# Optimization experiments

Hardware: AMD Instinct MI355X
Metric: run time of the kernel (lower is better)

Reference implementation:

```python
import jax, jax.numpy as jnp
import numpy as np


def setup_inputs() -> dict:
    key = jax.random.key(0)
    kq, kk, kv = jax.random.split(key, 3)
    # transpose_batch_sequence=True layout: [seq, batch, heads, head_dim]
    query = jax.random.normal(kq, (2048, 2, 32, 128), dtype=jnp.float32)
    k = jax.random.normal(kk, (2048, 2, 8, 128), dtype=jnp.float32)
    v = jax.random.normal(kv, (2048, 2, 8, 128), dtype=jnp.float32)
    return {"query": query, "key": k, "value": v}


def reference(query, key, value):
    # scale_attn_logits=True
    head_dim = query.shape[-1]
    q = query / jnp.sqrt(jnp.asarray(head_dim, dtype=query.dtype))
    h_q, h_kv = q.shape[-2], key.shape[-2]
    group_size = h_q // h_kv
    # [q, b, h_kv, g, d]
    gq = q.reshape((*q.shape[:2], h_kv, group_size, q.shape[-1]))
    # scores: [b, h_kv, g, q, k]
    attn = jnp.einsum('qbhgd,kbhd->bhgqk', gq, key)
    attn = jax.nn.softmax(attn, axis=-1)
    # output: [q, b, h_kv, g, d] -> [q, b, h_q, d]
    out = jnp.einsum('bhgqk,kbhd->qbhgd', attn, value)
    return out.reshape(query.shape)
```

## Files before the change

kernel.cpp:

```cpp
#include <hip/hip_runtime.h>

#define SEQ   2048
#define NB    2
#define NHQ   32
#define NHKV  8
#define HD    128
#define QTILE 256
#define QW    32
#define KVB   64
#define NWAVE 8
#define SCALE 0.08838834764831845f
#define QSCALE (0.08838834764831845f * 1.4426950408889634f)
#define THRL2 11.5f

#define QSTRIDE (NB * NHQ * HD)
#define KSTRIDE (NB * NHKV * HD)

typedef float f32x4  __attribute__((ext_vector_type(4)));
typedef float f32x16 __attribute__((ext_vector_type(16)));
typedef __bf16 bf16x8 __attribute__((ext_vector_type(8)));
typedef unsigned short ushort8 __attribute__((ext_vector_type(8)));
typedef unsigned int u32;
typedef unsigned int u32x2 __attribute__((ext_vector_type(2)));
typedef unsigned int u32x4 __attribute__((ext_vector_type(4)));

__device__ __forceinline__ unsigned short f2bf(float f) {
    union { float f; unsigned u; } c; c.f = f;
    return (unsigned short)((c.u + 0x7fffu + ((c.u >> 16) & 1u)) >> 16);
}

__device__ __forceinline__ void gload_lds16(const unsigned short* g, unsigned short* l) {
    __builtin_amdgcn_global_load_lds((const __attribute__((address_space(1))) u32*)g,
                                     (__attribute__((address_space(3))) u32*)l, 16, 0, 0);
}

__device__ __forceinline__ float ex2(float x) {
#if __has_builtin(__builtin_amdgcn_exp2f)
    return __builtin_amdgcn_exp2f(x);
#else
    return exp2f(x);
#endif
}

__device__ __forceinline__ u32 cvtpk(float lo, float hi) {
    u32 r;
    asm("v_cvt_pk_bf16_f32 %0, %1, %2" : "=v"(r) : "v"(lo), "v"(hi));
    return r;
}

__device__ __forceinline__ void pl32swap(u32& a, u32& b) {
#if __has_builtin(__builtin_amdgcn_permlane32_swap)
    u32x2 r = __builtin_amdgcn_permlane32_swap(a, b, false, false);
    a = r.x; b = r.y;
#else
    asm("v_permlane32_swap_b32 %0, %1" : "+v"(a), "+v"(b));
#endif
}

template <int B>
__device__ __forceinline__ bf16x8 make_pa(const f32x16 p) {
    u32 w0 = cvtpk(p[B + 0], p[B + 1]);
    u32 w2 = cvtpk(p[B + 4], p[B + 5]);
    pl32swap(w0, w2);
    u32 w1 = cvtpk(p[B + 2], p[B + 3]);
    u32 w3 = cvtpk(p[B + 6], p[B + 7]);
    pl32swap(w1, w3);
    u32x4 v = {w0, w1, w2, w3};
    return __builtin_bit_cast(bf16x8, v);
}

__global__ __launch_bounds__(256) void conv_k(const float* __restrict__ K,
                                              unsigned short* __restrict__ Kws) {
    int idx = blockIdx.x * 256 + threadIdx.x;
    int c  = idx & 15;
    int s  = (idx >> 4) & 2047;
    int bh = idx >> 15;
    int cs = c ^ (s & 7);
    const float* src = K + ((size_t)s * 16 + bh) * 128 + cs * 8;
    float4 f0 = *(const float4*)src;
    float4 f1 = *(const float4*)(src + 4);
    ushort8 u;
    u[0] = f2bf(f0.x); u[1] = f2bf(f0.y); u[2] = f2bf(f0.z); u[3] = f2bf(f0.w);
    u[4] = f2bf(f1.x); u[5] = f2bf(f1.y); u[6] = f2bf(f1.z); u[7] = f2bf(f1.w);
    *(ushort8*)&Kws[((size_t)bh * 2048 + s) * 128 + c * 8] = u;
}

__global__ __launch_bounds__(256) void conv_v(const float* __restrict__ V,
                                              unsigned short* __restrict__ Vt) {
    __shared__ float tile[64][129];
    int t64 = blockIdx.x & 31;
    int bh  = blockIdx.x >> 5;
    int kv0 = t64 * 64;
#pragma unroll
    for (int i = 0; i < 8; ++i) {
        int f4 = i * 256 + threadIdx.x;
        int kv = f4 >> 5, d4 = (f4 & 31) * 4;
        float4 v = *(const float4*)(V + ((size_t)(kv0 + kv) * 16 + bh) * 128 + d4);
        tile[kv][d4] = v.x; tile[kv][d4 + 1] = v.y;
        tile[kv][d4 + 2] = v.z; tile[kv][d4 + 3] = v.w;
    }
    __syncthreads();
#pragma unroll
    for (int i = 0; i < 4; ++i) {
        int lin = i * 256 + threadIdx.x;
        int c = lin & 7, d = lin >> 3;
        int cs = c ^ (d & 7);
        ushort8 u;
#pragma unroll
        for (int j = 0; j < 8; ++j) u[j] = f2bf(tile[cs * 8 + j][d]);
        *(ushort8*)&Vt[((size_t)bh * 128 + d) * 2048 + kv0 + c * 8] = u;
    }
}

__global__ __launch_bounds__(512, 2)
void attn_fwd3(const float* __restrict__ Q, const unsigned short* __restrict__ Kws,
               const unsigned short* __restrict__ Vtws, float* __restrict__ O) {
    __shared__ __align__(16) unsigned char smemc[69632];

    const int tid  = threadIdx.x;
    const int w    = tid >> 6;
    const int lane = tid & 63;
    const int q31  = lane & 31;
    const int h    = lane >> 5;
    const int c7   = q31 & 7;

    const int bid   = blockIdx.x;
    const int qtile = bid & 7;
    const int g     = (bid >> 3) & 3;
    const int b     = (bid >> 5) & 1;
    const int hkv   = bid >> 6;
    const int hq    = hkv * 4 + g;

    const int qrow = qtile * QTILE + w * QW + q31;

    bf16x8 qf[8];
    {
        const float* qp = Q + (size_t)qrow * QSTRIDE + b * (NHQ * HD) + hq * HD;
#pragma unroll
        for (int s = 0; s < 8; ++s) {
            const float* p = qp + (2 * s + h) * 8;
            float4 f0 = *(const float4*)(p);
            float4 f1 = *(const float4*)(p + 4);
            ushort8 u;
            u[0] = f2bf(f0.x * QSCALE); u[1] = f2bf(f0.y * QSCALE);
            u[2] = f2bf(f0.z * QSCALE); u[3] = f2bf(f0.w * QSCALE);
            u[4] = f2bf(f1.x * QSCALE); u[5] = f2bf(f1.y * QSCALE);
            u[6] = f2bf(f1.z * QSCALE); u[7] = f2bf(f1.w * QSCALE);
            qf[s] = __builtin_bit_cast(bf16x8, u);
        }
    }

    u32 kad[8], vad[4];
#pragma unroll
    for (int s = 0; s < 8; ++s)
        kad[s] = q31 * 256 + (((2 * s + h) ^ c7) << 4);
#pragma unroll
    for (int ks = 0; ks < 4; ++ks)
        vad[ks] = 32768 + q31 * 128 + (((2 * ks + h) ^ c7) << 4);

    f32x16 acc[4];
#pragma unroll
    for (int db = 0; db < 4; ++db) acc[db] = (f32x16)0.f;
    float mr = -3e38f, lsum = 0.f;

    const unsigned short* kbh = Kws  + (size_t)(b * 8 + hkv) * 2048 * 128;
    const unsigned short* vbh = Vtws + (size_t)(b * 8 + hkv) * 128 * 2048;

#define STAGE(bufi, tt) do {                                                           \
        const int kv0s = (tt) * KVB;                                                   \
        _Pragma("unroll")                                                              \
        for (int i_ = 0; i_ < 2; ++i_) {                                               \
            const int c_ = w * 2 + i_;                                                 \
            gload_lds16(kbh + (size_t)(kv0s + c_ * 4 + (lane >> 4)) * 128 + (lane & 15) * 8, \
                        (unsigned short*)(smemc + (bufi) * 16384 + c_ * 1024));        \
            gload_lds16(vbh + (size_t)(c_ * 8 + (lane >> 3)) * 2048 + kv0s + (lane & 7) * 8, \
                        (unsigned short*)(smemc + 32768 + (bufi) * 16384 + c_ * 1024)); \
        }                                                                              \
    } while (0)

    STAGE(0, 0);

    for (int t = 0; t < SEQ / KVB; ++t) {
        __syncthreads();
        if (t + 1 < SEQ / KVB) STAGE((t + 1) & 1, t + 1);

        f32x16 sa0 = (f32x16)0.f, sa1 = (f32x16)0.f;
#pragma unroll
        for (int s = 0; s < 8; ++s) {
            bf16x8 k0 = *(const bf16x8*)&smemc[kad[s]];
            bf16x8 k1 = *(const bf16x8*)&smemc[kad[s] + 8192];
            sa0 = __builtin_amdgcn_mfma_f32_32x32x16_bf16(k0, qf[s], sa0, 0, 0, 0);
            sa1 = __builtin_amdgcn_mfma_f32_32x32x16_bf16(k1, qf[s], sa1, 0, 0, 0);
        }

        float m4[4];
#pragma unroll
        for (int r = 0; r < 4; ++r)
            m4[r] = fmaxf(fmaxf(fmaxf(sa0[r], sa0[r + 4]), fmaxf(sa0[r + 8], sa0[r + 12])),
                          fmaxf(fmaxf(sa1[r], sa1[r + 4]), fmaxf(sa1[r + 8], sa1[r + 12])));
        float tm = fmaxf(fmaxf(m4[0], m4[1]), fmaxf(m4[2], m4[3]));
        tm = fmaxf(tm, __shfl_xor(tm, 32));

        if (!__all(tm <= mr + THRL2)) {
            float mn   = fmaxf(mr, tm);
            float corr = ex2(mr - mn);
            lsum *= corr;
#pragma unroll
            for (int db = 0; db < 4; ++db)
#pragma unroll
                for (int r = 0; r < 16; ++r) acc[db][r] *= corr;
            mr = mn;
        }

#pragma unroll
        for (int r = 0; r < 16; ++r) sa0[r] = ex2(sa0[r] - mr);
#pragma unroll
        for (int r = 0; r < 16; ++r) sa1[r] = ex2(sa1[r] - mr);
        float s4[4];
#pragma unroll
        for (int r = 0; r < 4; ++r)
            s4[r] = (sa0[r] + sa0[r + 4]) + (sa0[r + 8] + sa0[r + 12]) +
                    (sa1[r] + sa1[r + 4]) + (sa1[r + 8] + sa1[r + 12]);
        float ps = (s4[0] + s4[1]) + (s4[2] + s4[3]);
        ps += __shfl_xor(ps, 32);
        lsum += ps;

        bf16x8 pa[4];
        pa[0] = make_pa<0>(sa0);
        pa[1] = make_pa<8>(sa0);
        pa[2] = make_pa<0>(sa1);
        pa[3] = make_pa<8>(sa1);

#pragma unroll
        for (int db = 0; db < 4; ++db) {
#pragma unroll
            for (int ks = 0; ks < 4; ++ks) {
                bf16x8 vf = *(const bf16x8*)&smemc[vad[ks] + db * 4096];
                acc[db] = __builtin_amdgcn_mfma_f32_32x32x16_bf16(vf, pa[ks], acc[db], 0, 0, 0);
            }
        }

#pragma unroll
        for (int s = 0; s < 8; ++s) kad[s] ^= 16384;
#pragma unroll
        for (int ks = 0; ks < 4; ++ks) vad[ks] ^= 16384;
    }
#undef STAGE

    __syncthreads();
    float invl = 1.f / lsum;
    float* ep = (float*)(void*)smemc + w * 2176;
    const int qtb = qtile * QTILE + w * QW;
    float* ob = O + b * (NHQ * HD) + hq * HD;

#pragma unroll
    for (int pass = 0; pass < 2; ++pass) {
#pragma unroll
        for (int db2 = 0; db2 < 2; ++db2) {
            const int db = pass * 2 + db2;
#pragma unroll
            for (int r = 0; r < 16; ++r)
                ep[q31 * 68 + db2 * 32 + (r & 3) + 8 * (r >> 2) + 4 * h] = acc[db][r] * invl;
        }
        __syncthreads();
#pragma unroll
        for (int i = 0; i < 8; ++i) {
            const int row = i * 4 + (lane >> 4);
            const int f4  = lane & 15;
            float4 val = *(const float4*)&ep[row * 68 + f4 * 4];
            *(float4*)(ob + (size_t)(qtb + row) * QSTRIDE + pass * 64 + f4 * 4) = val;
        }
        __syncthreads();
    }
}

#define KPAD  136
#define VPAD  72
#define PPAD  72
__global__ __launch_bounds__(512, 2)
void attn_fwd(const float* __restrict__ Q, const float* __restrict__ K,
              const float* __restrict__ V, float* __restrict__ O) {
    __shared__ __align__(16) unsigned short kbuf[KVB * KPAD];
    __shared__ __align__(16) unsigned short vbuf[HD * VPAD];
    __shared__ __align__(16) unsigned short pbuf[NWAVE][16 * PPAD];

    const int tid = threadIdx.x;
    const int w = tid >> 6, lane = tid & 63;
    const int row16 = lane & 15, kg = lane >> 4;
    const int bid = blockIdx.x;
    const int qtile = bid & 7, g = (bid >> 3) & 3, b = (bid >> 5) & 1, hkv = bid >> 6;
    const int hq = hkv * 4 + g;
    const int qbase = qtile * QTILE + w * 32;

    ushort8 qf[2][4];
#pragma unroll
    for (int s = 0; s < 2; ++s) {
        const int qrow = qbase + s * 16 + row16;
        const float* qp = Q + (size_t)qrow * QSTRIDE + b * (NHQ * HD) + hq * HD;
#pragma unroll
        for (int kk = 0; kk < 4; ++kk) {
            const float* p = qp + kk * 32 + kg * 8;
            float4 f0 = *(const float4*)(p);
            float4 f1 = *(const float4*)(p + 4);
            ushort8 u;
            u[0] = f2bf(f0.x * SCALE); u[1] = f2bf(f0.y * SCALE);
            u[2] = f2bf(f0.z * SCALE); u[3] = f2bf(f0.w * SCALE);
            u[4] = f2bf(f1.x * SCALE); u[5] = f2bf(f1.y * SCALE);
            u[6] = f2bf(f1.z * SCALE); u[7] = f2bf(f1.w * SCALE);
            qf[s][kk] = u;
        }
    }
    float m[2][4], lsum[2][4];
    f32x4 acco[2][8];
#pragma unroll
    for (int s = 0; s < 2; ++s)
#pragma unroll
        for (int r = 0; r < 4; ++r) { m[s][r] = -1e30f; lsum[s][r] = 0.f; }
#pragma unroll
    for (int s = 0; s < 2; ++s)
#pragma unroll
        for (int n = 0; n < 8; ++n) acco[s][n] = (f32x4)0.f;

    const float* kb0 = K + b * (NHKV * HD) + hkv * HD;
    const float* vb0 = V + b * (NHKV * HD) + hkv * HD;

    for (int kvt = 0; kvt < SEQ / KVB; ++kvt) {
        const int kv0 = kvt * KVB;
        __syncthreads();
        const float* kb = kb0 + (size_t)kv0 * KSTRIDE;
#pragma unroll
        for (int i = 0; i < 2; ++i) {
            int c = i * 512 + tid;
            int row = c >> 4, c8 = c & 15;
            const float* src = kb + (size_t)row * KSTRIDE + c8 * 8;
            float4 f0 = *(const float4*)(src);
            float4 f1 = *(const float4*)(src + 4);
            ushort8 u;
            u[0] = f2bf(f0.x); u[1] = f2bf(f0.y); u[2] = f2bf(f0.z); u[3] = f2bf(f0.w);
            u[4] = f2bf(f1.x); u[5] = f2bf(f1.y); u[6] = f2bf(f1.z); u[7] = f2bf(f1.w);
            *(ushort8*)&kbuf[row * KPAD + c8 * 8] = u;
        }
        const float* vb = vb0 + (size_t)kv0 * KSTRIDE;
#pragma unroll
        for (int i = 0; i < 4; ++i) {
            int f4i = i * 512 + tid;
            int kv = f4i >> 5, d0 = (f4i & 31) * 4;
            float4 v4 = *(const float4*)(vb + (size_t)kv * KSTRIDE + d0);
            vbuf[(d0 + 0) * VPAD + kv] = f2bf(v4.x);
            vbuf[(d0 + 1) * VPAD + kv] = f2bf(v4.y);
            vbuf[(d0 + 2) * VPAD + kv] = f2bf(v4.z);
            vbuf[(d0 + 3) * VPAD + kv] = f2bf(v4.w);
        }
        __syncthreads();

        f32x4 sa[2][4];
#pragma unroll
        for (int s = 0; s < 2; ++s)
#pragma unroll
            for (int n = 0; n < 4; ++n) sa[s][n] = (f32x4)0.f;
#pragma unroll
        for (int kk = 0; kk < 4; ++kk) {
#pragma unroll
            for (int n = 0; n < 4; ++n) {
                bf16x8 bfr = *(const bf16x8*)&kbuf[(n * 16 + row16) * KPAD + kk * 32 + kg * 8];
                sa[0][n] = __builtin_amdgcn_mfma_f32_16x16x32_bf16(
                    __builtin_bit_cast(bf16x8, qf[0][kk]), bfr, sa[0][n], 0, 0, 0);
                sa[1][n] = __builtin_amdgcn_mfma_f32_16x16x32_bf16(
                    __builtin_bit_cast(bf16x8, qf[1][kk]), bfr, sa[1][n], 0, 0, 0);
            }
        }
#pragma unroll
        for (int s = 0; s < 2; ++s) {
#pragma unroll
            for (int r = 0; r < 4; ++r) {
                float tm = fmaxf(fmaxf(sa[s][0][r], sa[s][1][r]), fmaxf(sa[s][2][r], sa[s][3][r]));
                tm = fmaxf(tm, __shfl_xor(tm, 1, 16));
                tm = fmaxf(tm, __shfl_xor(tm, 2, 16));
                tm = fmaxf(tm, __shfl_xor(tm, 4, 16));
                tm = fmaxf(tm, __shfl_xor(tm, 8, 16));
                float mn = fmaxf(m[s][r], tm);
                float corr = __expf(m[s][r] - mn);
                float ps = 0.f;
                int prow = kg * 4 + r;
#pragma unroll
                for (int n = 0; n < 4; ++n) {
                    float p = __expf(sa[s][n][r] - mn);
                    ps += p;
                    pbuf[w][prow * PPAD + n * 16 + row16] = f2bf(p);
                }
                ps += __shfl_xor(ps, 1, 16);
                ps += __shfl_xor(ps, 2, 16);
                ps += __shfl_xor(ps, 4, 16);
                ps += __shfl_xor(ps, 8, 16);
                lsum[s][r] = lsum[s][r] * corr + ps;
                m[s][r] = mn;
#pragma unroll
                for (int n8 = 0; n8 < 8; ++n8) acco[s][n8][r] *= corr;
            }
#pragma unroll
            for (int kk2 = 0; kk2 < 2; ++kk2) {
                bf16x8 pa = *(const bf16x8*)&pbuf[w][row16 * PPAD + kk2 * 32 + kg * 8];
#pragma unroll
                for (int n8 = 0; n8 < 8; ++n8) {
                    bf16x8 vf = *(const bf16x8*)&vbuf[(n8 * 16 + row16) * VPAD + kk2 * 32 + kg * 8];
                    acco[s][n8] = __builtin_amdgcn_mfma_f32_16x16x32_bf16(pa, vf, acco[s][n8], 0, 0, 0);
                }
            }
        }
    }
    float* ob = O + b * (NHQ * HD) + hq * HD;
#pragma unroll
    for (int s = 0; s < 2; ++s)
#pragma unroll
        for (int r = 0; r < 4; ++r) {
            float inv = 1.f / lsum[s][r];
            int qrow = qbase + s * 16 + kg * 4 + r;
            float* op = ob + (size_t)qrow * QSTRIDE;
#pragma unroll
            for (int n8 = 0; n8 < 8; ++n8)
                op[n8 * 16 + row16] = acco[s][n8][r] * inv;
        }
}

extern "C" void kernel_launch(void* const* d_in, const int* in_sizes, int n_in,
                              void* d_out, int out_size, void* d_ws, size_t ws_size,
                              hipStream_t stream) {
    (void)in_sizes; (void)n_in; (void)out_size;
    const float* Q = (const float*)d_in[0];
    const float* K = (const float*)d_in[1];
    const float* V = (const float*)d_in[2];
    float* Out = (float*)d_out;

    const size_t kv_elems = (size_t)16 * 2048 * 128;
    const size_t need = kv_elems * 2 * sizeof(unsigned short);

    if (ws_size >= need) {
        unsigned short* Kws = (unsigned short*)d_ws;
        unsigned short* Vt  = Kws + kv_elems;
        conv_k<<<dim3(2048), dim3(256), 0, stream>>>(K, Kws);
        conv_v<<<dim3(512), dim3(256), 0, stream>>>(V, Vt);
        attn_fwd3<<<dim3(512), dim3(512), 0, stream>>>(Q, Kws, Vt, Out);
    } else {
        attn_fwd<<<dim3(512), dim3(512), 0, stream>>>(Q, K, V, Out);
    }
}
```

Baseline: 170.6 us.

## Process two 32-row query sub-tiles per wave to reuse K/V LDS fragments

Each wave now handles 64 query rows as two 32-row halves with separate accumulators and softmax state, so every K and V fragment read from LDS feeds two MFMAs. The grid shrinks to 256 blocks, and block IDs are remapped so heads sharing a KV stream are adjacent. The loop is split into two 32-column KV halves with s_setprio around the MFMA bursts, and the cross-half row-sum reduction moves to the end. In exchange, register pressure roughly doubles under launch_bounds(512,2), and the smaller grid may under-fill the 256 CUs.

Result: slower. 202.1 us (+18.5%).

```diff
diff --git a/kernel.cpp b/kernel.cpp
--- a/kernel.cpp
+++ b/kernel.cpp
@@ -5,8 +5,8 @@
 #define NHQ   32
 #define NHKV  8
 #define HD    128
-#define QTILE 256
-#define QW    32
+#define QTILE 512
+#define QW    64
 #define KVB   64
 #define NWAVE 8
 #define SCALE 0.08838834764831845f
@@ -113,7 +113,7 @@
 }
 
 __global__ __launch_bounds__(512, 2)
-void attn_fwd3(const float* __restrict__ Q, const unsigned short* __restrict__ Kws,
+void attn_fwd4(const float* __restrict__ Q, const unsigned short* __restrict__ Kws,
                const unsigned short* __restrict__ Vtws, float* __restrict__ O) {
     __shared__ __align__(16) unsigned char smemc[69632];
 
@@ -125,17 +125,19 @@
     const int c7   = q31 & 7;
 
     const int bid   = blockIdx.x;
-    const int qtile = bid & 7;
-    const int g     = (bid >> 3) & 3;
-    const int b     = (bid >> 5) & 1;
-    const int hkv   = bid >> 6;
+    const int hkv   = bid & 7;
+    const int rest  = bid >> 3;
+    const int g     = rest & 3;
+    const int b     = (rest >> 2) & 1;
+    const int qtile = rest >> 3;
     const int hq    = hkv * 4 + g;
 
-    const int qrow = qtile * QTILE + w * QW + q31;
-
-    bf16x8 qf[8];
-    {
-        const float* qp = Q + (size_t)qrow * QSTRIDE + b * (NHQ * HD) + hq * HD;
+    const int qbase = qtile * QTILE + w * QW;
+
+    bf16x8 qfa[8], qfb[8];
+#pragma unroll
+    for (int qs = 0; qs < 2; ++qs) {
+        const float* qp = Q + (size_t)(qbase + qs * 32 + q31) * QSTRIDE + b * (NHQ * HD) + hq * HD;
 #pragma unroll
         for (int s = 0; s < 8; ++s) {
             const float* p = qp + (2 * s + h) * 8;
@@ -146,7 +148,8 @@
             u[2] = f2bf(f0.z * QSCALE); u[3] = f2bf(f0.w * QSCALE);
             u[4] = f2bf(f1.x * QSCALE); u[5] = f2bf(f1.y * QSCALE);
             u[6] = f2bf(f1.z * QSCALE); u[7] = f2bf(f1.w * QSCALE);
-            qf[s] = __builtin_bit_cast(bf16x8, u);
+            if (qs == 0) qfa[s] = __builtin_bit_cast(bf16x8, u);
+            else         qfb[s] = __builtin_bit_cast(bf16x8, u);
         }
     }
 
@@ -158,10 +161,10 @@
     for (int ks = 0; ks < 4; ++ks)
         vad[ks] = 32768 + q31 * 128 + (((2 * ks + h) ^ c7) << 4);
 
-    f32x16 acc[4];
-#pragma unroll
-    for (int db = 0; db < 4; ++db) acc[db] = (f32x16)0.f;
-    float mr = -3e38f, lsum = 0.f;
+    f32x16 acca[4], accb[4];
+#pragma unroll
+    for (int db = 0; db < 4; ++db) { acca[db] = (f32x16)0.f; accb[db] = (f32x16)0.f; }
+    float mra = -3e38f, lsa = 0.f, mrb = -3e38f, lsb = 0.f;
 
     const unsigned short* kbh = Kws  + (size_t)(b * 8 + hkv) * 2048 * 128;
     const unsigned short* vbh = Vtws + (size_t)(b * 8 + hkv) * 128 * 2048;
@@ -184,60 +187,84 @@
         __syncthreads();
         if (t + 1 < SEQ / KVB) STAGE((t + 1) & 1, t + 1);
 
-        f32x16 sa0 = (f32x16)0.f, sa1 = (f32x16)0.f;
-#pragma unroll
-        for (int s = 0; s < 8; ++s) {
-            bf16x8 k0 = *(const bf16x8*)&smemc[kad[s]];
-            bf16x8 k1 = *(const bf16x8*)&smemc[kad[s] + 8192];
-            sa0 = __builtin_amdgcn_mfma_f32_32x32x16_bf16(k0, qf[s], sa0, 0, 0, 0);
-            sa1 = __builtin_amdgcn_mfma_f32_32x32x16_bf16(k1, qf[s], sa1, 0, 0, 0);
-        }
-
-        float m4[4];
-#pragma unroll
-        for (int r = 0; r < 4; ++r)
-            m4[r] = fmaxf(fmaxf(fmaxf(sa0[r], sa0[r + 4]), fmaxf(sa0[r + 8], sa0[r + 12])),
-                          fmaxf(fmaxf(sa1[r], sa1[r + 4]), fmaxf(sa1[r + 8], sa1[r + 12])));
-        float tm = fmaxf(fmaxf(m4[0], m4[1]), fmaxf(m4[2], m4[3]));
-        tm = fmaxf(tm, __shfl_xor(tm, 32));
-
-        if (!__all(tm <= mr + THRL2)) {
-            float mn   = fmaxf(mr, tm);
-            float corr = ex2(mr - mn);
-            lsum *= corr;
-#pragma unroll
-            for (int db = 0; db < 4; ++db)
-#pragma unroll
-                for (int r = 0; r < 16; ++r) acc[db][r] *= corr;
-            mr = mn;
-        }
-
-#pragma unroll
-        for (int r = 0; r < 16; ++r) sa0[r] = ex2(sa0[r] - mr);
-#pragma unroll
-        for (int r = 0; r < 16; ++r) sa1[r] = ex2(sa1[r] - mr);
-        float s4[4];
-#pragma unroll
-        for (int r = 0; r < 4; ++r)
-            s4[r] = (sa0[r] + sa0[r + 4]) + (sa0[r + 8] + sa0[r + 12]) +
-                    (sa1[r] + sa1[r + 4]) + (sa1[r + 8] + sa1[r + 12]);
-        float ps = (s4[0] + s4[1]) + (s4[2] + s4[3]);
-        ps += __shfl_xor(ps, 32);
-        lsum += ps;
-
-        bf16x8 pa[4];
-        pa[0] = make_pa<0>(sa0);
-        pa[1] = make_pa<8>(sa0);
-        pa[2] = make_pa<0>(sa1);
-        pa[3] = make_pa<8>(sa1);
-
-#pragma unroll
-        for (int db = 0; db < 4; ++db) {
-#pragma unroll
-            for (int ks = 0; ks < 4; ++ks) {
-                bf16x8 vf = *(const bf16x8*)&smemc[vad[ks] + db * 4096];
-                acc[db] = __builtin_amdgcn_mfma_f32_32x32x16_bf16(vf, pa[ks], acc[db], 0, 0, 0);
-            }
+#pragma unroll
+        for (int X = 0; X < 2; ++X) {
+            f32x16 saa = (f32x16)0.f, sab = (f32x16)0.f;
+            __builtin_amdgcn_s_setprio(1);
+#pragma unroll
+            for (int s = 0; s < 8; ++s) {
+                bf16x8 kf = *(const bf16x8*)&smemc[kad[s] + X * 8192];
+                saa = __builtin_amdgcn_mfma_f32_32x32x16_bf16(kf, qfa[s], saa, 0, 0, 0);
+                sab = __builtin_amdgcn_mfma_f32_32x32x16_bf16(kf, qfb[s], sab, 0, 0, 0);
+            }
+            __builtin_amdgcn_s_setprio(0);
+
+            {
+                float t0 = fmaxf(fmaxf(saa[0], saa[1]),  fmaxf(saa[2], saa[3]));
+                float t1 = fmaxf(fmaxf(saa[4], saa[5]),  fmaxf(saa[6], saa[7]));
+                float t2 = fmaxf(fmaxf(saa[8], saa[9]),  fmaxf(saa[10], saa[11]));
+                float t3 = fmaxf(fmaxf(saa[12], saa[13]), fmaxf(saa[14], saa[15]));
+                float tm = fmaxf(fmaxf(t0, t1), fmaxf(t2, t3));
+                tm = fmaxf(tm, __shfl_xor(tm, 32));
+                if (!__all(tm <= mra + THRL2)) {
+                    float mn = fmaxf(mra, tm);
+                    float corr = ex2(mra - mn);
+                    lsa *= corr;
+#pragma unroll
+                    for (int db = 0; db < 4; ++db)
+#pragma unroll
+                        for (int r = 0; r < 16; ++r) acca[db][r] *= corr;
+                    mra = mn;
+                }
+#pragma unroll
+                for (int r = 0; r < 16; ++r) saa[r] = ex2(saa[r] - mra);
+                float s0 = (saa[0] + saa[1]) + (saa[2] + saa[3]);
+                float s1 = (saa[4] + saa[5]) + (saa[6] + saa[7]);
+                float s2 = (saa[8] + saa[9]) + (saa[10] + saa[11]);
+                float s3 = (saa[12] + saa[13]) + (saa[14] + saa[15]);
+                lsa += (s0 + s1) + (s2 + s3);
+            }
+            {
+                float t0 = fmaxf(fmaxf(sab[0], sab[1]),  fmaxf(sab[2], sab[3]));
+                float t1 = fmaxf(fmaxf(sab[4], sab[5]),  fmaxf(sab[6], sab[7]));
+                float t2 = fmaxf(fmaxf(sab[8], sab[9]),  fmaxf(sab[10], sab[11]));
+                float t3 = fmaxf(fmaxf(sab[12], sab[13]), fmaxf(sab[14], sab[15]));
+                float tm = fmaxf(fmaxf(t0, t1), fmaxf(t2, t3));
+                tm = fmaxf(tm, __shfl_xor(tm, 32));
+                if (!__all(tm <= mrb + THRL2)) {
+                    float mn = fmaxf(mrb, tm);
+                    float corr = ex2(mrb - mn);
+                    lsb *= corr;
+#pragma unroll
+                    for (int db = 0; db < 4; ++db)
+#pragma unroll
+                        for (int r = 0; r < 16; ++r) accb[db][r] *= corr;
+                    mrb = mn;
+                }
+#pragma unroll
+                for (int r = 0; r < 16; ++r) sab[r] = ex2(sab[r] - mrb);
+                float s0 = (sab[0] + sab[1]) + (sab[2] + sab[3]);
+                float s1 = (sab[4] + sab[5]) + (sab[6] + sab[7]);
+                float s2 = (sab[8] + sab[9]) + (sab[10] + sab[11]);
+                float s3 = (sab[12] + sab[13]) + (sab[14] + sab[15]);
+                lsb += (s0 + s1) + (s2 + s3);
+            }
+
+            bf16x8 paa[2], pab[2];
+            paa[0] = make_pa<0>(saa); paa[1] = make_pa<8>(saa);
+            pab[0] = make_pa<0>(sab); pab[1] = make_pa<8>(sab);
+
+            __builtin_amdgcn_s_setprio(1);
+#pragma unroll
+            for (int db = 0; db < 4; ++db) {
+#pragma unroll
+                for (int ks = 0; ks < 2; ++ks) {
+                    bf16x8 vf = *(const bf16x8*)&smemc[vad[2 * X + ks] + db * 4096];
+                    acca[db] = __builtin_amdgcn_mfma_f32_32x32x16_bf16(vf, paa[ks], acca[db], 0, 0, 0);
+                    accb[db] = __builtin_amdgcn_mfma_f32_32x32x16_bf16(vf, pab[ks], accb[db], 0, 0, 0);
+                }
+            }
+            __builtin_amdgcn_s_setprio(0);
         }
 
 #pragma unroll
@@ -248,29 +275,37 @@
 #undef STAGE
 
     __syncthreads();
-    float invl = 1.f / lsum;
+    lsa += __shfl_xor(lsa, 32);
+    lsb += __shfl_xor(lsb, 32);
+    float invla = 1.f / lsa, invlb = 1.f / lsb;
     float* ep = (float*)(void*)smemc + w * 2176;
-    const int qtb = qtile * QTILE + w * QW;
     float* ob = O + b * (NHQ * HD) + hq * HD;
 
 #pragma unroll
-    for (int pass = 0; pass < 2; ++pass) {
-#pragma unroll
-        for (int db2 = 0; db2 < 2; ++db2) {
-            const int db = pass * 2 + db2;
-#pragma unroll
-            for (int r = 0; r < 16; ++r)
-                ep[q31 * 68 + db2 * 32 + (r & 3) + 8 * (r >> 2) + 4 * h] = acc[db][r] * invl;
-        }
-        __syncthreads();
-#pragma unroll
-        for (int i = 0; i < 8; ++i) {
-            const int row = i * 4 + (lane >> 4);
-            const int f4  = lane & 15;
-            float4 val = *(const float4*)&ep[row * 68 + f4 * 4];
-            *(float4*)(ob + (size_t)(qtb + row) * QSTRIDE + pass * 64 + f4 * 4) = val;
-        }
-        __syncthreads();
+    for (int qs = 0; qs < 2; ++qs) {
+        const int qtb = qbase + qs * 32;
+        const float invl = qs ? invlb : invla;
+#pragma unroll
+        for (int pass = 0; pass < 2; ++pass) {
+#pragma unroll
+            for (int db2 = 0; db2 < 2; ++db2) {
+                const int db = pass * 2 + db2;
+#pragma unroll
+                for (int r = 0; r < 16; ++r) {
+                    float v = (qs ? accb[db][r] : acca[db][r]) * invl;
+                    ep[q31 * 68 + db2 * 32 + (r & 3) + 8 * (r >> 2) + 4 * h] = v;
+                }
+            }
+            __syncthreads();
+#pragma unroll
+            for (int i = 0; i < 8; ++i) {
+                const int row = i * 4 + (lane >> 4);
+                const int f4  = lane & 15;
+                float4 val = *(const float4*)&ep[row * 68 + f4 * 4];
+                *(float4*)(ob + (size_t)(qtb + row) * QSTRIDE + pass * 64 + f4 * 4) = val;
+            }
+            __syncthreads();
+        }
     }
 }
 
@@ -290,7 +325,7 @@
     const int bid = blockIdx.x;
     const int qtile = bid & 7, g = (bid >> 3) & 3, b = (bid >> 5) & 1, hkv = bid >> 6;
     const int hq = hkv * 4 + g;
-    const int qbase = qtile * QTILE + w * 32;
+    const int qbase = qtile * 256 + w * 32;
 
     ushort8 qf[2][4];
 #pragma unroll
@@ -439,7 +474,7 @@
         unsigned short* Vt  = Kws + kv_elems;
         conv_k<<<dim3(2048), dim3(256), 0, stream>>>(K, Kws);
         conv_v<<<dim3(512), dim3(256), 0, stream>>>(V, Vt);
-        attn_fwd3<<<dim3(512), dim3(512), 0, stream>>>(Q, Kws, Vt, Out);
+        attn_fwd4<<<dim3(256), dim3(512), 0, stream>>>(Q, Kws, Vt, Out);
     } else {
         attn_fwd<<<dim3(512), dim3(512), 0, stream>>>(Q, K, V, Out);
     }
```

## Triple-buffer K/V LDS staging with explicit vmcnt waits and MFMA priority

Applied to the files above, without the earlier changes.

The attention kernel moves from double to triple-buffered LDS staging of K and V, prefetching two tiles ahead and replacing __syncthreads with an explicit vmcnt wait plus s_barrier so loads can stay in flight across iterations. MFMA sections are wrapped in s_setprio to favor matrix issue, and block indices are remapped so hkv varies fastest, which may improve L2 sharing of K/V across concurrent blocks. The larger LDS footprint (96KB) and launch_bounds(512,1) cut occupancy to one block per CU, trading latency hiding across blocks for deeper in-block pipelining.

New measurement: 174.3 us. 2.2% more time.

```diff
diff --git a/kernel.cpp b/kernel.cpp
--- a/kernel.cpp
+++ b/kernel.cpp
@@ -8,7 +8,7 @@
 #define QTILE 256
 #define QW    32
 #define KVB   64
-#define NWAVE 8
+#define NT    (SEQ / KVB)
 #define SCALE 0.08838834764831845f
 #define QSCALE (0.08838834764831845f * 1.4426950408889634f)
 #define THRL2 11.5f
@@ -112,10 +112,10 @@
     }
 }
 
-__global__ __launch_bounds__(512, 2)
-void attn_fwd3(const float* __restrict__ Q, const unsigned short* __restrict__ Kws,
+__global__ __launch_bounds__(512, 1)
+void attn_fwd6(const float* __restrict__ Q, const unsigned short* __restrict__ Kws,
                const unsigned short* __restrict__ Vtws, float* __restrict__ O) {
-    __shared__ __align__(16) unsigned char smemc[69632];
+    __shared__ __align__(16) unsigned char smemc[98304];
 
     const int tid  = threadIdx.x;
     const int w    = tid >> 6;
@@ -125,10 +125,11 @@
     const int c7   = q31 & 7;
 
     const int bid   = blockIdx.x;
-    const int qtile = bid & 7;
-    const int g     = (bid >> 3) & 3;
-    const int b     = (bid >> 5) & 1;
-    const int hkv   = bid >> 6;
+    const int hkv   = bid & 7;
+    const int rest  = bid >> 3;
+    const int g     = rest & 3;
+    const int b     = (rest >> 2) & 1;
+    const int qtile = rest >> 3;
     const int hq    = hkv * 4 + g;
 
     const int qrow = qtile * QTILE + w * QW + q31;
@@ -156,7 +157,7 @@
         kad[s] = q31 * 256 + (((2 * s + h) ^ c7) << 4);
 #pragma unroll
     for (int ks = 0; ks < 4; ++ks)
-        vad[ks] = 32768 + q31 * 128 + (((2 * ks + h) ^ c7) << 4);
+        vad[ks] = 49152 + q31 * 128 + (((2 * ks + h) ^ c7) << 4);
 
     f32x16 acc[4];
 #pragma unroll
@@ -166,32 +167,42 @@
     const unsigned short* kbh = Kws  + (size_t)(b * 8 + hkv) * 2048 * 128;
     const unsigned short* vbh = Vtws + (size_t)(b * 8 + hkv) * 128 * 2048;
 
-#define STAGE(bufi, tt) do {                                                           \
+#define STAGE(sofb, tt) do {                                                           \
         const int kv0s = (tt) * KVB;                                                   \
         _Pragma("unroll")                                                              \
         for (int i_ = 0; i_ < 2; ++i_) {                                               \
             const int c_ = w * 2 + i_;                                                 \
             gload_lds16(kbh + (size_t)(kv0s + c_ * 4 + (lane >> 4)) * 128 + (lane & 15) * 8, \
-                        (unsigned short*)(smemc + (bufi) * 16384 + c_ * 1024));        \
+                        (unsigned short*)(smemc + (sofb) + c_ * 1024));                \
             gload_lds16(vbh + (size_t)(c_ * 8 + (lane >> 3)) * 2048 + kv0s + (lane & 7) * 8, \
-                        (unsigned short*)(smemc + 32768 + (bufi) * 16384 + c_ * 1024)); \
+                        (unsigned short*)(smemc + 49152 + (sofb) + c_ * 1024));        \
         }                                                                              \
     } while (0)
 
     STAGE(0, 0);
-
-    for (int t = 0; t < SEQ / KVB; ++t) {
-        __syncthreads();
-        if (t + 1 < SEQ / KVB) STAGE((t + 1) & 1, t + 1);
+    STAGE(16384, 1);
+    int kof = 0;
+    int sof = 32768;
+
+    for (int t = 0; t < NT; ++t) {
+        if (t < NT - 1) {
+            asm volatile("s_waitcnt vmcnt(4)" ::: "memory");
+        } else {
+            asm volatile("s_waitcnt vmcnt(0)" ::: "memory");
+        }
+        __builtin_amdgcn_s_barrier();
+        if (t + 2 < NT) STAGE(sof, t + 2);
 
         f32x16 sa0 = (f32x16)0.f, sa1 = (f32x16)0.f;
+        __builtin_amdgcn_s_setprio(1);
 #pragma unroll
         for (int s = 0; s < 8; ++s) {
-            bf16x8 k0 = *(const bf16x8*)&smemc[kad[s]];
-            bf16x8 k1 = *(const bf16x8*)&smemc[kad[s] + 8192];
+            bf16x8 k0 = *(const bf16x8*)&smemc[kad[s] + kof];
+            bf16x8 k1 = *(const bf16x8*)&smemc[kad[s] + kof + 8192];
             sa0 = __builtin_amdgcn_mfma_f32_32x32x16_bf16(k0, qf[s], sa0, 0, 0, 0);
             sa1 = __builtin_amdgcn_mfma_f32_32x32x16_bf16(k1, qf[s], sa1, 0, 0, 0);
         }
+        __builtin_amdgcn_s_setprio(0);
 
         float m4[4];
 #pragma unroll
@@ -231,19 +242,19 @@
         pa[2] = make_pa<0>(sa1);
         pa[3] = make_pa<8>(sa1);
 
+        __builtin_amdgcn_s_setprio(1);
 #pragma unroll
         for (int db = 0; db < 4; ++db) {
 #pragma unroll
             for (int ks = 0; ks < 4; ++ks) {
-                bf16x8 vf = *(const bf16x8*)&smemc[vad[ks] + db * 4096];
+                bf16x8 vf = *(const bf16x8*)&smemc[vad[ks] + kof + db * 4096];
                 acc[db] = __builtin_amdgcn_mfma_f32_32x32x16_bf16(vf, pa[ks], acc[db], 0, 0, 0);
             }
         }
-
-#pragma unroll
-        for (int s = 0; s < 8; ++s) kad[s] ^= 16384;
-#pragma unroll
-        for (int ks = 0; ks < 4; ++ks) vad[ks] ^= 16384;
+        __builtin_amdgcn_s_setprio(0);
+
+        kof = (kof == 32768) ? 0 : kof + 16384;
+        sof = (sof == 32768) ? 0 : sof + 16384;
     }
 #undef STAGE
 
@@ -282,7 +293,7 @@
               const float* __restrict__ V, float* __restrict__ O) {
     __shared__ __align__(16) unsigned short kbuf[KVB * KPAD];
     __shared__ __align__(16) unsigned short vbuf[HD * VPAD];
-    __shared__ __align__(16) unsigned short pbuf[NWAVE][16 * PPAD];
+    __shared__ __align__(16) unsigned short pbuf[8][16 * PPAD];
 
     const int tid = threadIdx.x;
     const int w = tid >> 6, lane = tid & 63;
@@ -290,7 +301,7 @@
     const int bid = blockIdx.x;
     const int qtile = bid & 7, g = (bid >> 3) & 3, b = (bid >> 5) & 1, hkv = bid >> 6;
     const int hq = hkv * 4 + g;
-    const int qbase = qtile * QTILE + w * 32;
+    const int qbase = qtile * 256 + w * 32;
 
     ushort8 qf[2][4];
 #pragma unroll
@@ -439,7 +450,7 @@
         unsigned short* Vt  = Kws + kv_elems;
         conv_k<<<dim3(2048), dim3(256), 0, stream>>>(K, Kws);
         conv_v<<<dim3(512), dim3(256), 0, stream>>>(V, Vt);
-        attn_fwd3<<<dim3(512), dim3(512), 0, stream>>>(Q, Kws, Vt, Out);
+        attn_fwd6<<<dim3(512), dim3(512), 0, stream>>>(Q, Kws, Vt, Out);
     } else {
         attn_fwd<<<dim3(512), dim3(512), 0, stream>>>(Q, K, V, Out);
     }
```
